# Kernel optimization log

Hardware: AMD Instinct MI355X
Metric: run time of the kernel (lower is better)

## Reference

```python
import jax, jax.numpy as jnp
import numpy as np

N = 100000   # nodes
E = 1600000  # edges (avg degree 16)
D = 64
L = 4        # layers per GNN stack


def setup_inputs() -> dict:
    key = jax.random.key(0)
    ks = jax.random.split(key, 16)
    s = 0.125  # ~kaiming scale for fan_in=64
    return {
        "x": jax.random.normal(ks[0], (N, D), jnp.float32),
        "edge_index": jax.random.randint(ks[1], (2, E), 0, N, dtype=jnp.int32),
        "sage_Wl": jax.random.normal(ks[2], (L, D, D), jnp.float32) * s,
        "sage_bl": jnp.zeros((L, D), jnp.float32),
        "sage_Wr": jax.random.normal(ks[3], (L, D, D), jnp.float32) * s,
        "gat_W": jax.random.normal(ks[4], (L, D, D), jnp.float32) * s,
        "gat_asrc": jax.random.normal(ks[5], (L, D), jnp.float32) * s,
        "gat_adst": jax.random.normal(ks[6], (L, D), jnp.float32) * s,
        "gat_b": jnp.zeros((L, D), jnp.float32),
        "proj_W1": jax.random.normal(ks[7], (64, 64), jnp.float32) * s,
        "proj_b1": jnp.zeros((64,), jnp.float32),
        "proj_W2": jax.random.normal(ks[8], (32, 64), jnp.float32) * s,
        "proj_b2": jnp.zeros((32,), jnp.float32),
        "proj_W3": jax.random.normal(ks[9], (16, 32), jnp.float32) * (0.25 ** 0.5),
        "proj_b3": jnp.zeros((16,), jnp.float32),
    }


def _sage_conv(x, Wl, bl, Wr, src, dst, n):
    # out_i = Wl @ mean_{j in N(i)} x_j + bl + Wr @ x_i
    msg_sum = jax.ops.segment_sum(x[src], dst, num_segments=n)
    deg = jax.ops.segment_sum(jnp.ones(src.shape[0], x.dtype), dst, num_segments=n)
    mean = msg_sum / jnp.maximum(deg, 1.0)[:, None]
    return mean @ Wl.T + bl + x @ Wr.T


def _gat_conv(x, W, a_src, a_dst, b, src_sl, dst_sl, n):
    # single-head GATConv with self-loops (src_sl/dst_sl include them)
    h = x @ W.T                      # [N, D]
    alpha_s = h @ a_src              # [N]
    alpha_d = h @ a_dst              # [N]
    e = jax.nn.leaky_relu(alpha_s[src_sl] + alpha_d[dst_sl], 0.2)  # [E+N]
    m = jax.ops.segment_max(e, dst_sl, num_segments=n)
    p = jnp.exp(e - m[dst_sl])
    z = jax.ops.segment_sum(p, dst_sl, num_segments=n)
    alpha = p / z[dst_sl]
    out = jax.ops.segment_sum(alpha[:, None] * h[src_sl], dst_sl, num_segments=n)
    return out + b


def reference(x, edge_index, sage_Wl, sage_bl, sage_Wr,
              gat_W, gat_asrc, gat_adst, gat_b,
              proj_W1, proj_b1, proj_W2, proj_b2, proj_W3, proj_b3):
    n = x.shape[0]
    src, dst = edge_index[0], edge_index[1]
    loops = jnp.arange(n, dtype=edge_index.dtype)
    src_sl = jnp.concatenate([src, loops])
    dst_sl = jnp.concatenate([dst, loops])

    h = x
    for i in range(L):  # GraphSAGE: ReLU between layers, none after last
        h = _sage_conv(h, sage_Wl[i], sage_bl[i], sage_Wr[i], src, dst, n)
        if i < L - 1:
            h = jax.nn.relu(h)
    for i in range(L):  # GAT
        h = _gat_conv(h, gat_W[i], gat_asrc[i], gat_adst[i], gat_b[i], src_sl, dst_sl, n)
        if i < L - 1:
            h = jax.nn.relu(h)

    # Projection MLP (Dropout inactive at inference)
    h = jax.nn.relu(h @ proj_W1.T + proj_b1)
    h = jax.nn.relu(h @ proj_W2.T + proj_b2)
    return h @ proj_W3.T + proj_b3
```

## Files before the change

### kernel.cpp

```cpp
#include <hip/hip_runtime.h>
#include <hip/hip_fp16.h>

#define D 64
#define D4 16
#define PITCH 68
#define HP 36

typedef float4 f4;
typedef unsigned int u32;
typedef __attribute__((ext_vector_type(4))) _Float16 f16x4;
typedef __attribute__((ext_vector_type(4))) float f32x4;

__device__ __forceinline__ float leaky02(float x) { return (x >= 0.f) ? x : 0.2f * x; }

__device__ __forceinline__ f4 f4add(f4 a, f4 b) {
    return make_float4(a.x + b.x, a.y + b.y, a.z + b.z, a.w + b.w);
}
__device__ __forceinline__ f4 f4fma(float s, f4 v, f4 a) {
    return make_float4(fmaf(s, v.x, a.x), fmaf(s, v.y, a.y), fmaf(s, v.z, a.z), fmaf(s, v.w, a.w));
}
__device__ __forceinline__ f4 f4scale(f4 a, float s) {
    return make_float4(a.x * s, a.y * s, a.z * s, a.w * s);
}

__device__ __forceinline__ u32 pack2(float a, float b) {
    __half2 h = __floats2half2_rn(a, b);
    return *reinterpret_cast<u32*>(&h);
}
__device__ __forceinline__ uint2 pack4(float a, float b, float c, float d) {
    uint2 u;
    u.x = pack2(a, b);
    u.y = pack2(c, d);
    return u;
}
__device__ __forceinline__ f4 h2f4(uint2 u) {
    __half2 ha = *reinterpret_cast<__half2*>(&u.x);
    __half2 hb = *reinterpret_cast<__half2*>(&u.y);
    float2 fa = __half22float2(ha);
    float2 fb = __half22float2(hb);
    return make_float4(fa.x, fa.y, fb.x, fb.y);
}


__global__ __launch_bounds__(256) void hist_kernel(const int* __restrict__ dst,
                                                   int* __restrict__ cnt, int ne) {
    int e = blockIdx.x * blockDim.x + threadIdx.x;
    if (e < ne) atomicAdd(&cnt[dst[e]], 1);
}

#define SCAN_BS 256
__global__ __launch_bounds__(SCAN_BS) void scan1_kernel(const int* __restrict__ cnt,
                                                        int* __restrict__ incl,
                                                        int* __restrict__ partials, int n) {
    __shared__ int sm[SCAN_BS];
    int g = blockIdx.x * SCAN_BS + threadIdx.x;
    int v = (g < n) ? cnt[g] : 0;
    sm[threadIdx.x] = v;
    __syncthreads();
    for (int off = 1; off < SCAN_BS; off <<= 1) {
        int t = (threadIdx.x >= off) ? sm[threadIdx.x - off] : 0;
        __syncthreads();
        sm[threadIdx.x] += t;
        __syncthreads();
    }
    if (g < n) incl[g] = sm[threadIdx.x];
    if (threadIdx.x == SCAN_BS - 1) partials[blockIdx.x] = sm[threadIdx.x];
}

__global__ __launch_bounds__(1024) void scan2_kernel(int* __restrict__ partials, int nb) {
    __shared__ int sm[1024];
    int t = threadIdx.x;
    int v = (t < nb) ? partials[t] : 0;
    sm[t] = v;
    __syncthreads();
    for (int off = 1; off < 1024; off <<= 1) {
        int x = (t >= off) ? sm[t - off] : 0;
        __syncthreads();
        sm[t] += x;
        __syncthreads();
    }
    if (t < nb) partials[t] = sm[t] - v;
}

__global__ __launch_bounds__(SCAN_BS) void scan3_kernel(const int* __restrict__ cnt,
                                                        const int* __restrict__ incl,
                                                        const int* __restrict__ partials,
                                                        int* __restrict__ rowptr,
                                                        int* __restrict__ cursor, int n, int ne) {
    int g = blockIdx.x * SCAN_BS + threadIdx.x;
    if (g < n) {
        int rp = incl[g] - cnt[g] + partials[blockIdx.x];
        rowptr[g] = rp;
        cursor[g] = rp;
    }
    if (g == 0) rowptr[n] = ne;
}

__global__ __launch_bounds__(256) void fill_kernel(const int* __restrict__ src,
                                                   const int* __restrict__ dst,
                                                   int* __restrict__ cursor,
                                                   int* __restrict__ col, int ne) {
    int e = blockIdx.x * blockDim.x + threadIdx.x;
    if (e < ne) {
        int pos = atomicAdd(&cursor[dst[e]], 1);
        col[pos] = src[e];
    }
}


__global__ __launch_bounds__(256) void to_half(const float* __restrict__ in,
                                               uint2* __restrict__ out, int total4) {
    int i = blockIdx.x * 256 + threadIdx.x;
    if (i < total4) {
        f4 v = *(const f4*)&in[i * 4];
        out[i] = pack4(v.x, v.y, v.z, v.w);
    }
}


__device__ __forceinline__ void stage_h32(u32* __restrict__ T, const f4* __restrict__ G4,
                                          int t, int valid_rows) {
    int row = t >> 2, q = t & 3;
#pragma unroll
    for (int c = 0; c < 4; c++) {
        int kq = q + 4 * c;
        f4 r = make_float4(0.f, 0.f, 0.f, 0.f);
        if (row < valid_rows) r = G4[(size_t)row * 16 + kq];
        uint2 p = pack4(r.x, r.y, r.z, r.w);
        T[row * HP + kq * 2] = p.x;
        T[row * HP + kq * 2 + 1] = p.y;
    }
}

__device__ __forceinline__ f16x4 ldfrag(const u32* __restrict__ T, int row, int kidx) {
    uint2 v;
    v.x = T[row * HP + kidx * 2];
    v.y = T[row * HP + kidx * 2 + 1];
    return __builtin_bit_cast(f16x4, v);
}


__device__ __forceinline__ void stageT(float* __restrict__ T, const f4* __restrict__ G4,
                                       int t, int valid_rows) {
    int row = t >> 2;
    int kq0 = t & 3;
#pragma unroll
    for (int c = 0; c < 4; c++) {
        int kq = kq0 + 4 * c;
        f4 r = make_float4(0.f, 0.f, 0.f, 0.f);
        if (row < valid_rows) r = G4[(size_t)row * 16 + kq];
        int k0 = kq * 4;
        T[(k0 + 0) * PITCH + row] = r.x;
        T[(k0 + 1) * PITCH + row] = r.y;
        T[(k0 + 2) * PITCH + row] = r.z;
        T[(k0 + 3) * PITCH + row] = r.w;
    }
}

#define TILE_MM(At, Wt, acc, r, c, KDIM)                                      \
    for (int k = 0; k < KDIM; k++) {                                          \
        f4 a = *(const f4*)&(At)[k * PITCH + (r) * 4];                        \
        f4 w = *(const f4*)&(Wt)[k * PITCH + (c) * 4];                        \
        acc[0][0] = fmaf(a.x, w.x, acc[0][0]);                                \
        acc[0][1] = fmaf(a.x, w.y, acc[0][1]);                                \
        acc[0][2] = fmaf(a.x, w.z, acc[0][2]);                                \
        acc[0][3] = fmaf(a.x, w.w, acc[0][3]);                                \
        acc[1][0] = fmaf(a.y, w.x, acc[1][0]);                                \
        acc[1][1] = fmaf(a.y, w.y, acc[1][1]);                                \
        acc[1][2] = fmaf(a.y, w.z, acc[1][2]);                                \
        acc[1][3] = fmaf(a.y, w.w, acc[1][3]);                                \
        acc[2][0] = fmaf(a.z, w.x, acc[2][0]);                                \
        acc[2][1] = fmaf(a.z, w.y, acc[2][1]);                                \
        acc[2][2] = fmaf(a.z, w.z, acc[2][2]);                                \
        acc[2][3] = fmaf(a.z, w.w, acc[2][3]);                                \
        acc[3][0] = fmaf(a.w, w.x, acc[3][0]);                                \
        acc[3][1] = fmaf(a.w, w.y, acc[3][1]);                                \
        acc[3][2] = fmaf(a.w, w.z, acc[3][2]);                                \
        acc[3][3] = fmaf(a.w, w.w, acc[3][3]);                                \
    }


__global__ __launch_bounds__(256) void sage_gather(const uint2* __restrict__ Hh,
                                                   const int* __restrict__ rowptr,
                                                   const int* __restrict__ col,
                                                   f4* __restrict__ M, int n) {
    int lane = threadIdx.x & 63;
    int eg = lane >> 4, l16 = lane & 15;
    int wave = (blockIdx.x * 256 + threadIdx.x) >> 6;
    int nw = (gridDim.x * 256) >> 6;
    for (int node = wave; node < n; node += nw) {
        int start = rowptr[node], end = rowptr[node + 1];
        int len = end - start;
        f4 a0 = {0, 0, 0, 0}, a1 = {0, 0, 0, 0}, a2 = {0, 0, 0, 0}, a3 = {0, 0, 0, 0};
        int main16 = len & ~15;
        int o = 0;
        for (; o < main16; o += 16) {
            int i0 = start + o + eg;
            int s0 = col[i0];
            int s1 = col[i0 + 4];
            int s2 = col[i0 + 8];
            int s3 = col[i0 + 12];
            uint2 v0 = Hh[(size_t)s0 * D4 + l16];
            uint2 v1 = Hh[(size_t)s1 * D4 + l16];
            uint2 v2 = Hh[(size_t)s2 * D4 + l16];
            uint2 v3 = Hh[(size_t)s3 * D4 + l16];
            a0 = f4add(a0, h2f4(v0)); a1 = f4add(a1, h2f4(v1));
            a2 = f4add(a2, h2f4(v2)); a3 = f4add(a3, h2f4(v3));
        }
        int rem = len - o;
        if (rem > 0) {
            int i0 = start + o;
            if (eg < rem)      a0 = f4add(a0, h2f4(Hh[(size_t)col[i0 + eg] * D4 + l16]));
            if (eg + 4 < rem)  a1 = f4add(a1, h2f4(Hh[(size_t)col[i0 + 4 + eg] * D4 + l16]));
            if (eg + 8 < rem)  a2 = f4add(a2, h2f4(Hh[(size_t)col[i0 + 8 + eg] * D4 + l16]));
            if (eg + 12 < rem) a3 = f4add(a3, h2f4(Hh[(size_t)col[i0 + 12 + eg] * D4 + l16]));
        }
        f4 a = f4add(f4add(a0, a1), f4add(a2, a3));
        a.x += __shfl_xor(a.x, 16); a.y += __shfl_xor(a.y, 16);
        a.z += __shfl_xor(a.z, 16); a.w += __shfl_xor(a.w, 16);
        a.x += __shfl_xor(a.x, 32); a.y += __shfl_xor(a.y, 32);
        a.z += __shfl_xor(a.z, 32); a.w += __shfl_xor(a.w, 32);
        if (eg == 0) {
            float invd = 1.f / fmaxf((float)len, 1.f);
            M[(size_t)node * D4 + l16] =
                make_float4(a.x * invd, a.y * invd, a.z * invd, a.w * invd);
        }
    }
}


__global__ __launch_bounds__(256) void sage_dense_mfma(const f4* __restrict__ M4,
                                                       const f4* __restrict__ h4,
                                                       const float* __restrict__ Wl,
                                                       const float* __restrict__ bl,
                                                       const float* __restrict__ Wr,
                                                       float* __restrict__ outf,
                                                       u32* __restrict__ outh32,
                                                       int relu_flag, int n) {
    __shared__ __align__(16) u32 Ah[64 * HP];
    __shared__ __align__(16) u32 Bh[64 * HP];
    int t = threadIdx.x;
    int nb = blockIdx.x * 64;
    int w = t >> 6, l = t & 63;
    int lr = l & 15, g = l >> 4;
    f32x4 acc[4] = {{0, 0, 0, 0}, {0, 0, 0, 0}, {0, 0, 0, 0}, {0, 0, 0, 0}};
    stage_h32(Ah, M4 + (size_t)nb * 16, t, n - nb);
    stage_h32(Bh, (const f4*)Wl, t, 64);
    __syncthreads();
#pragma unroll
    for (int kb = 0; kb < 4; kb++) {
        f16x4 af = ldfrag(Ah, w * 16 + lr, kb * 4 + g);
#pragma unroll
        for (int ob = 0; ob < 4; ob++) {
            f16x4 bf = ldfrag(Bh, ob * 16 + lr, kb * 4 + g);
            acc[ob] = __builtin_amdgcn_mfma_f32_16x16x16f16(af, bf, acc[ob], 0, 0, 0);
        }
    }
    __syncthreads();
    stage_h32(Ah, h4 + (size_t)nb * 16, t, n - nb);
    stage_h32(Bh, (const f4*)Wr, t, 64);
    __syncthreads();
#pragma unroll
    for (int kb = 0; kb < 4; kb++) {
        f16x4 af = ldfrag(Ah, w * 16 + lr, kb * 4 + g);
#pragma unroll
        for (int ob = 0; ob < 4; ob++) {
            f16x4 bf = ldfrag(Bh, ob * 16 + lr, kb * 4 + g);
            acc[ob] = __builtin_amdgcn_mfma_f32_16x16x16f16(af, bf, acc[ob], 0, 0, 0);
        }
    }
#pragma unroll
    for (int ob = 0; ob < 4; ob++) {
        int colx = ob * 16 + lr;
        float bv = bl[colx];
#pragma unroll
        for (int j = 0; j < 4; j++) {
            int row = w * 16 + 4 * g + j;
            int node = nb + row;
            float v = acc[ob][j] + bv;
            if (relu_flag) v = fmaxf(v, 0.f);
            float vup = __shfl_down(v, 1);
            if (node < n) {
                outf[(size_t)node * 64 + colx] = v;
                if ((lr & 1) == 0) outh32[(size_t)node * 32 + (colx >> 1)] = pack2(v, vup);
            }
        }
    }
}


__global__ __launch_bounds__(256) void gat_transform_mfma(const f4* __restrict__ h4,
                                                          const float* __restrict__ W,
                                                          const float* __restrict__ a_src,
                                                          const float* __restrict__ a_dst,
                                                          u32* __restrict__ hth32,
                                                          float* __restrict__ as_,
                                                          float* __restrict__ ad_, int n) {
    __shared__ __align__(16) u32 Ah[64 * HP];
    __shared__ __align__(16) u32 Bh[64 * HP];
    int t = threadIdx.x;
    int nb = blockIdx.x * 64;
    int w = t >> 6, l = t & 63;
    int lr = l & 15, g = l >> 4;
    f32x4 acc[4] = {{0, 0, 0, 0}, {0, 0, 0, 0}, {0, 0, 0, 0}, {0, 0, 0, 0}};
    stage_h32(Ah, h4 + (size_t)nb * 16, t, n - nb);
    stage_h32(Bh, (const f4*)W, t, 64);
    __syncthreads();
#pragma unroll
    for (int kb = 0; kb < 4; kb++) {
        f16x4 af = ldfrag(Ah, w * 16 + lr, kb * 4 + g);
#pragma unroll
        for (int ob = 0; ob < 4; ob++) {
            f16x4 bf = ldfrag(Bh, ob * 16 + lr, kb * 4 + g);
            acc[ob] = __builtin_amdgcn_mfma_f32_16x16x16f16(af, bf, acc[ob], 0, 0, 0);
        }
    }
    float asv[4], adv[4];
#pragma unroll
    for (int ob = 0; ob < 4; ob++) {
        asv[ob] = a_src[ob * 16 + lr];
        adv[ob] = a_dst[ob * 16 + lr];
    }
#pragma unroll
    for (int j = 0; j < 4; j++) {
        int row = w * 16 + 4 * g + j;
        int node = nb + row;
        float ps = 0.f, pd = 0.f;
#pragma unroll
        for (int ob = 0; ob < 4; ob++) {
            ps = fmaf(acc[ob][j], asv[ob], ps);
            pd = fmaf(acc[ob][j], adv[ob], pd);
        }
#pragma unroll
        for (int off = 1; off < 16; off <<= 1) {
            ps += __shfl_xor(ps, off);
            pd += __shfl_xor(pd, off);
        }
        if (lr == 0 && node < n) {
            as_[node] = ps;
            ad_[node] = pd;
        }
#pragma unroll
        for (int ob = 0; ob < 4; ob++) {
            int colx = ob * 16 + lr;
            float v = acc[ob][j];
            float vup = __shfl_down(v, 1);
            if (node < n && (lr & 1) == 0)
                hth32[(size_t)node * 32 + (colx >> 1)] = pack2(v, vup);
        }
    }
}


__global__ __launch_bounds__(256) void gat_gather(const int* __restrict__ rowptr,
                                                  const int* __restrict__ col,
                                                  const float* __restrict__ as_,
                                                  const float* __restrict__ ad_,
                                                  const uint2* __restrict__ Hh,
                                                  const float* __restrict__ b,
                                                  f4* __restrict__ out,
                                                  int relu_flag, int n) {
    int lane = threadIdx.x & 63;
    int eg = lane >> 4, l16 = lane & 15;
    int wave = (blockIdx.x * 256 + threadIdx.x) >> 6;
    int nw = (gridDim.x * 256) >> 6;
    const f4* b4 = (const f4*)b;
    for (int node = wave; node < n; node += nw) {
        int start = rowptr[node], end = rowptr[node + 1];
        int len = end - start;
        float ad_n = ad_[node];
        float e_self = leaky02(as_[node] + ad_n);
        float m = e_self;
        float zp = (eg == 0) ? 1.f : 0.f;
        f4 acc = {0, 0, 0, 0};
        if (eg == 0) acc = h2f4(Hh[(size_t)node * D4 + l16]);
        int main16 = len & ~15;
        int o = 0;
        for (; o < main16; o += 16) {
            int i0 = start + o + eg;
            int s0 = col[i0];
            int s1 = col[i0 + 4];
            int s2 = col[i0 + 8];
            int s3 = col[i0 + 12];
            uint2 v0 = Hh[(size_t)s0 * D4 + l16];
            uint2 v1 = Hh[(size_t)s1 * D4 + l16];
            uint2 v2 = Hh[(size_t)s2 * D4 + l16];
            uint2 v3 = Hh[(size_t)s3 * D4 + l16];
            float e0 = leaky02(as_[s0] + ad_n);
            float e1 = leaky02(as_[s1] + ad_n);
            float e2 = leaky02(as_[s2] + ad_n);
            float e3 = leaky02(as_[s3] + ad_n);
            float em = fmaxf(fmaxf(e0, e1), fmaxf(e2, e3));
            em = fmaxf(em, __shfl_xor(em, 16));
            em = fmaxf(em, __shfl_xor(em, 32));
            if (em > m) {
                float sc = __expf(m - em);
                zp *= sc;
                acc = f4scale(acc, sc);
                m = em;
            }
            float p0 = __expf(e0 - m);
            float p1 = __expf(e1 - m);
            float p2 = __expf(e2 - m);
            float p3 = __expf(e3 - m);
            zp += (p0 + p1) + (p2 + p3);
            acc = f4fma(p0, h2f4(v0), acc);
            acc = f4fma(p1, h2f4(v1), acc);
            acc = f4fma(p2, h2f4(v2), acc);
            acc = f4fma(p3, h2f4(v3), acc);
        }
        int rem = len - o;
        if (rem > 0) {
            int i0 = start + o;
            bool v0b = eg < rem, v1b = eg + 4 < rem, v2b = eg + 8 < rem, v3b = eg + 12 < rem;
            int s0 = v0b ? col[i0 + eg] : 0;
            int s1 = v1b ? col[i0 + 4 + eg] : 0;
            int s2 = v2b ? col[i0 + 8 + eg] : 0;
            int s3 = v3b ? col[i0 + 12 + eg] : 0;
            float e0 = v0b ? leaky02(as_[s0] + ad_n) : -3.4e38f;
            float e1 = v1b ? leaky02(as_[s1] + ad_n) : -3.4e38f;
            float e2 = v2b ? leaky02(as_[s2] + ad_n) : -3.4e38f;
            float e3 = v3b ? leaky02(as_[s3] + ad_n) : -3.4e38f;
            float em = fmaxf(fmaxf(e0, e1), fmaxf(e2, e3));
            em = fmaxf(em, __shfl_xor(em, 16));
            em = fmaxf(em, __shfl_xor(em, 32));
            if (em > m) {
                float sc = __expf(m - em);
                zp *= sc;
                acc = f4scale(acc, sc);
                m = em;
            }
            float p0 = v0b ? __expf(e0 - m) : 0.f;
            float p1 = v1b ? __expf(e1 - m) : 0.f;
            float p2 = v2b ? __expf(e2 - m) : 0.f;
            float p3 = v3b ? __expf(e3 - m) : 0.f;
            zp += (p0 + p1) + (p2 + p3);
            if (v0b) acc = f4fma(p0, h2f4(Hh[(size_t)s0 * D4 + l16]), acc);
            if (v1b) acc = f4fma(p1, h2f4(Hh[(size_t)s1 * D4 + l16]), acc);
            if (v2b) acc = f4fma(p2, h2f4(Hh[(size_t)s2 * D4 + l16]), acc);
            if (v3b) acc = f4fma(p3, h2f4(Hh[(size_t)s3 * D4 + l16]), acc);
        }
        float z = zp;
        z += __shfl_xor(z, 16);
        z += __shfl_xor(z, 32);
        acc.x += __shfl_xor(acc.x, 16); acc.y += __shfl_xor(acc.y, 16);
        acc.z += __shfl_xor(acc.z, 16); acc.w += __shfl_xor(acc.w, 16);
        acc.x += __shfl_xor(acc.x, 32); acc.y += __shfl_xor(acc.y, 32);
        acc.z += __shfl_xor(acc.z, 32); acc.w += __shfl_xor(acc.w, 32);
        if (eg == 0) {
            float rz = 1.f / z;
            f4 bb = b4[l16];
            f4 o4 = make_float4(fmaf(acc.x, rz, bb.x), fmaf(acc.y, rz, bb.y),
                                fmaf(acc.z, rz, bb.z), fmaf(acc.w, rz, bb.w));
            if (relu_flag) {
                o4.x = fmaxf(o4.x, 0.f); o4.y = fmaxf(o4.y, 0.f);
                o4.z = fmaxf(o4.z, 0.f); o4.w = fmaxf(o4.w, 0.f);
            }
            out[(size_t)node * D4 + l16] = o4;
        }
    }
}


__global__ __launch_bounds__(256) void mlp_kernel(const f4* __restrict__ h4,
                                                  const float* __restrict__ W1,
                                                  const float* __restrict__ b1,
                                                  const float* __restrict__ W2,
                                                  const float* __restrict__ b2,
                                                  const float* __restrict__ W3,
                                                  const float* __restrict__ b3,
                                                  float* __restrict__ out, int n) {
    __shared__ float At[64 * PITCH];
    __shared__ float Wt[64 * PITCH];
    __shared__ float V2[32 * PITCH];
    int t = threadIdx.x;
    int nb = blockIdx.x * 64;
    int r = t >> 4, c = t & 15;
    stageT(At, h4 + (size_t)nb * 16, t, n - nb);
    stageT(Wt, (const f4*)W1, t, 64);
    __syncthreads();
    float a1v[4][4] = {{0.f}};
    TILE_MM(At, Wt, a1v, r, c, 64)
    f4 b1v = ((const f4*)b1)[c];
    __syncthreads();
    {
        float bb[4] = {b1v.x, b1v.y, b1v.z, b1v.w};
#pragma unroll
        for (int i = 0; i < 4; i++)
#pragma unroll
            for (int j = 0; j < 4; j++)
                At[(c * 4 + j) * PITCH + r * 4 + i] = fmaxf(a1v[i][j] + bb[j], 0.f);
    }
    stageT(Wt, (const f4*)W2, t, 32);
    __syncthreads();
    float a2v[4][2] = {{0.f}};
    for (int k = 0; k < 64; k++) {
        f4 a = *(const f4*)&At[k * PITCH + r * 4];
        float w0 = Wt[k * PITCH + c * 2];
        float w1 = Wt[k * PITCH + c * 2 + 1];
        a2v[0][0] = fmaf(a.x, w0, a2v[0][0]); a2v[0][1] = fmaf(a.x, w1, a2v[0][1]);
        a2v[1][0] = fmaf(a.y, w0, a2v[1][0]); a2v[1][1] = fmaf(a.y, w1, a2v[1][1]);
        a2v[2][0] = fmaf(a.z, w0, a2v[2][0]); a2v[2][1] = fmaf(a.z, w1, a2v[2][1]);
        a2v[3][0] = fmaf(a.w, w0, a2v[3][0]); a2v[3][1] = fmaf(a.w, w1, a2v[3][1]);
    }
    float b20 = b2[c * 2], b21 = b2[c * 2 + 1];
    __syncthreads();
#pragma unroll
    for (int i = 0; i < 4; i++) {
        V2[(c * 2 + 0) * PITCH + r * 4 + i] = fmaxf(a2v[i][0] + b20, 0.f);
        V2[(c * 2 + 1) * PITCH + r * 4 + i] = fmaxf(a2v[i][1] + b21, 0.f);
    }
    if (t < 128) {
        int row = t >> 3, kq = t & 7;
        f4 w = ((const f4*)W3)[row * 8 + kq];
        int k0 = kq * 4;
        Wt[(k0 + 0) * PITCH + row] = w.x;
        Wt[(k0 + 1) * PITCH + row] = w.y;
        Wt[(k0 + 2) * PITCH + row] = w.z;
        Wt[(k0 + 3) * PITCH + row] = w.w;
    }
    __syncthreads();
    float a3v[4] = {0.f, 0.f, 0.f, 0.f};
    for (int k = 0; k < 32; k++) {
        f4 a = *(const f4*)&V2[k * PITCH + r * 4];
        float w = Wt[k * PITCH + c];
        a3v[0] = fmaf(a.x, w, a3v[0]);
        a3v[1] = fmaf(a.y, w, a3v[1]);
        a3v[2] = fmaf(a.z, w, a3v[2]);
        a3v[3] = fmaf(a.w, w, a3v[3]);
    }
    float b3v = b3[c];
#pragma unroll
    for (int i = 0; i < 4; i++) {
        int node = nb + r * 4 + i;
        if (node < n) out[(size_t)node * 16 + c] = a3v[i] + b3v;
    }
}


extern "C" void kernel_launch(void* const* d_in, const int* in_sizes, int n_in,
                              void* d_out, int out_size, void* d_ws, size_t ws_size,
                              hipStream_t stream) {
    const int n  = in_sizes[0] / D;
    const int ne = in_sizes[1] / 2;

    const float* x        = (const float*)d_in[0];
    const int*   ei       = (const int*)d_in[1];
    const int*   src      = ei;
    const int*   dst      = ei + ne;
    const float* sage_Wl  = (const float*)d_in[2];
    const float* sage_bl  = (const float*)d_in[3];
    const float* sage_Wr  = (const float*)d_in[4];
    const float* gat_W    = (const float*)d_in[5];
    const float* gat_asrc = (const float*)d_in[6];
    const float* gat_adst = (const float*)d_in[7];
    const float* gat_b    = (const float*)d_in[8];
    const float* W1 = (const float*)d_in[9];
    const float* b1 = (const float*)d_in[10];
    const float* W2 = (const float*)d_in[11];
    const float* b2 = (const float*)d_in[12];
    const float* W3 = (const float*)d_in[13];
    const float* b3 = (const float*)d_in[14];
    float* out = (float*)d_out;

    int*   cnt      = (int*)d_ws;
    int*   incl     = cnt + n;
    int*   rowptr   = incl + n;
    int*   cursor   = rowptr + n + 4;
    int*   partials = cursor + n;
    int*   col      = partials + 1024;
    float* as_      = (float*)(col + ne);
    float* ad_      = as_ + n;
    float* M        = ad_ + n;
    float* bufA     = M + (size_t)n * D;
    float* bufB     = bufA + (size_t)n * D;
    uint2* Hh       = (uint2*)(bufB + (size_t)n * D);

    const int gridE  = (ne + 255) / 256;
    const int nb     = (n + SCAN_BS - 1) / SCAN_BS;
    const int gridG  = 4096;
    const int gridM  = (n + 63) / 64;
    const int gridC  = (n * D / 4 + 255) / 256;

    hipMemsetAsync(cnt, 0, (size_t)n * 4, stream);
    hist_kernel<<<gridE, 256, 0, stream>>>(dst, cnt, ne);
    scan1_kernel<<<nb, SCAN_BS, 0, stream>>>(cnt, incl, partials, n);
    scan2_kernel<<<1, 1024, 0, stream>>>(partials, nb);
    scan3_kernel<<<nb, SCAN_BS, 0, stream>>>(cnt, incl, partials, rowptr, cursor, n, ne);
    fill_kernel<<<gridE, 256, 0, stream>>>(src, dst, cursor, col, ne);

    to_half<<<gridC, 256, 0, stream>>>(x, Hh, n * D / 4);
    const float* cur = x;
    float* nxt = bufA;
    for (int l = 0; l < 4; l++) {
        sage_gather<<<gridG, 256, 0, stream>>>(Hh, rowptr, col, (f4*)M, n);
        sage_dense_mfma<<<gridM, 256, 0, stream>>>((const f4*)M, (const f4*)cur,
                                                   sage_Wl + (size_t)l * D * D,
                                                   sage_bl + (size_t)l * D,
                                                   sage_Wr + (size_t)l * D * D,
                                                   nxt, (u32*)Hh, (l < 3) ? 1 : 0, n);
        cur = nxt;
        nxt = (nxt == bufA) ? bufB : bufA;
    }

    float* gin = bufB;
    for (int l = 0; l < 4; l++) {
        gat_transform_mfma<<<gridM, 256, 0, stream>>>((const f4*)gin,
                                                      gat_W + (size_t)l * D * D,
                                                      gat_asrc + (size_t)l * D,
                                                      gat_adst + (size_t)l * D,
                                                      (u32*)Hh, as_, ad_, n);
        gat_gather<<<gridG, 256, 0, stream>>>(rowptr, col, as_, ad_,
                                              Hh, gat_b + (size_t)l * D, (f4*)gin,
                                              (l < 3) ? 1 : 0, n);
    }

    mlp_kernel<<<gridM, 256, 0, stream>>>((const f4*)gin, W1, b1, W2, b2, W3, b3, out, n);
}
```

Measured before the change: 869.0 us.

## Fuse SAGE neighbor gather with MFMA dense transform via LDS staging

Merges the SAGE mean-aggregation gather and the MFMA dense layer into one kernel. Each wave gathers 16 nodes and writes the fp16 mean straight into shared memory instead of round-tripping an fp32 M buffer through global memory. The fp16 feature buffer is now double-buffered (A/B ping-pong) so that blocks reading neighbors never race with blocks writing outputs. This also drops one launch per layer. In exchange the gather runs with a fixed per-block node assignment instead of a grid-stride loop over more waves, which may reduce latency hiding and load balance.

```diff
diff --git a/kernel.cpp b/kernel.cpp
--- a/kernel.cpp
+++ b/kernel.cpp
@@ -180,15 +180,36 @@
     }
 
 
-__global__ __launch_bounds__(256) void sage_gather(const uint2* __restrict__ Hh,
-                                                   const int* __restrict__ rowptr,
-                                                   const int* __restrict__ col,
-                                                   f4* __restrict__ M, int n) {
-    int lane = threadIdx.x & 63;
-    int eg = lane >> 4, l16 = lane & 15;
-    int wave = (blockIdx.x * 256 + threadIdx.x) >> 6;
-    int nw = (gridDim.x * 256) >> 6;
-    for (int node = wave; node < n; node += nw) {
+__global__ __launch_bounds__(256) void sage_fused(const uint2* __restrict__ Hh_in,
+                                                  const f4* __restrict__ h4,
+                                                  const int* __restrict__ rowptr,
+                                                  const int* __restrict__ col,
+                                                  const float* __restrict__ Wl,
+                                                  const float* __restrict__ bl,
+                                                  const float* __restrict__ Wr,
+                                                  float* __restrict__ outf,
+                                                  u32* __restrict__ Hh_out,
+                                                  int relu_flag, int n) {
+    __shared__ __align__(16) u32 Ah[64 * HP];
+    __shared__ __align__(16) u32 Bh[64 * HP];
+    int t = threadIdx.x;
+    int nb = blockIdx.x * 64;
+    int w = t >> 6, l = t & 63;
+    int lr = l & 15, g = l >> 4;
+    int eg = l >> 4, l16 = l & 15;
+
+    stage_h32(Bh, (const f4*)Wl, t, 64);
+
+    for (int i = 0; i < 16; i++) {
+        int row = w * 16 + i;
+        int node = nb + row;
+        if (node >= n) {
+            if (eg == 0) {
+                Ah[row * HP + l16 * 2] = 0u;
+                Ah[row * HP + l16 * 2 + 1] = 0u;
+            }
+            continue;
+        }
         int start = rowptr[node], end = rowptr[node + 1];
         int len = end - start;
         f4 a0 = {0, 0, 0, 0}, a1 = {0, 0, 0, 0}, a2 = {0, 0, 0, 0}, a3 = {0, 0, 0, 0};
@@ -200,20 +221,20 @@
             int s1 = col[i0 + 4];
             int s2 = col[i0 + 8];
             int s3 = col[i0 + 12];
-            uint2 v0 = Hh[(size_t)s0 * D4 + l16];
-            uint2 v1 = Hh[(size_t)s1 * D4 + l16];
-            uint2 v2 = Hh[(size_t)s2 * D4 + l16];
-            uint2 v3 = Hh[(size_t)s3 * D4 + l16];
+            uint2 v0 = Hh_in[(size_t)s0 * D4 + l16];
+            uint2 v1 = Hh_in[(size_t)s1 * D4 + l16];
+            uint2 v2 = Hh_in[(size_t)s2 * D4 + l16];
+            uint2 v3 = Hh_in[(size_t)s3 * D4 + l16];
             a0 = f4add(a0, h2f4(v0)); a1 = f4add(a1, h2f4(v1));
             a2 = f4add(a2, h2f4(v2)); a3 = f4add(a3, h2f4(v3));
         }
         int rem = len - o;
         if (rem > 0) {
             int i0 = start + o;
-            if (eg < rem)      a0 = f4add(a0, h2f4(Hh[(size_t)col[i0 + eg] * D4 + l16]));
-            if (eg + 4 < rem)  a1 = f4add(a1, h2f4(Hh[(size_t)col[i0 + 4 + eg] * D4 + l16]));
-            if (eg + 8 < rem)  a2 = f4add(a2, h2f4(Hh[(size_t)col[i0 + 8 + eg] * D4 + l16]));
-            if (eg + 12 < rem) a3 = f4add(a3, h2f4(Hh[(size_t)col[i0 + 12 + eg] * D4 + l16]));
+            if (eg < rem)      a0 = f4add(a0, h2f4(Hh_in[(size_t)col[i0 + eg] * D4 + l16]));
+            if (eg + 4 < rem)  a1 = f4add(a1, h2f4(Hh_in[(size_t)col[i0 + 4 + eg] * D4 + l16]));
+            if (eg + 8 < rem)  a2 = f4add(a2, h2f4(Hh_in[(size_t)col[i0 + 8 + eg] * D4 + l16]));
+            if (eg + 12 < rem) a3 = f4add(a3, h2f4(Hh_in[(size_t)col[i0 + 12 + eg] * D4 + l16]));
         }
         f4 a = f4add(f4add(a0, a1), f4add(a2, a3));
         a.x += __shfl_xor(a.x, 16); a.y += __shfl_xor(a.y, 16);
@@ -222,31 +243,13 @@
         a.z += __shfl_xor(a.z, 32); a.w += __shfl_xor(a.w, 32);
         if (eg == 0) {
             float invd = 1.f / fmaxf((float)len, 1.f);
-            M[(size_t)node * D4 + l16] =
-                make_float4(a.x * invd, a.y * invd, a.z * invd, a.w * invd);
-        }
-    }
-}
-
-
-__global__ __launch_bounds__(256) void sage_dense_mfma(const f4* __restrict__ M4,
-                                                       const f4* __restrict__ h4,
-                                                       const float* __restrict__ Wl,
-                                                       const float* __restrict__ bl,
-                                                       const float* __restrict__ Wr,
-                                                       float* __restrict__ outf,
-                                                       u32* __restrict__ outh32,
-                                                       int relu_flag, int n) {
-    __shared__ __align__(16) u32 Ah[64 * HP];
-    __shared__ __align__(16) u32 Bh[64 * HP];
-    int t = threadIdx.x;
-    int nb = blockIdx.x * 64;
-    int w = t >> 6, l = t & 63;
-    int lr = l & 15, g = l >> 4;
+            Ah[row * HP + l16 * 2] = pack2(a.x * invd, a.y * invd);
+            Ah[row * HP + l16 * 2 + 1] = pack2(a.z * invd, a.w * invd);
+        }
+    }
+    __syncthreads();
+
     f32x4 acc[4] = {{0, 0, 0, 0}, {0, 0, 0, 0}, {0, 0, 0, 0}, {0, 0, 0, 0}};
-    stage_h32(Ah, M4 + (size_t)nb * 16, t, n - nb);
-    stage_h32(Bh, (const f4*)Wl, t, 64);
-    __syncthreads();
 #pragma unroll
     for (int kb = 0; kb < 4; kb++) {
         f16x4 af = ldfrag(Ah, w * 16 + lr, kb * 4 + g);
@@ -282,7 +285,7 @@
             float vup = __shfl_down(v, 1);
             if (node < n) {
                 outf[(size_t)node * 64 + colx] = v;
-                if ((lr & 1) == 0) outh32[(size_t)node * 32 + (colx >> 1)] = pack2(v, vup);
+                if ((lr & 1) == 0) Hh_out[(size_t)node * 32 + (colx >> 1)] = pack2(v, vup);
             }
         }
     }
@@ -571,10 +574,10 @@
     int*   col      = partials + 1024;
     float* as_      = (float*)(col + ne);
     float* ad_      = as_ + n;
-    float* M        = ad_ + n;
-    float* bufA     = M + (size_t)n * D;
+    float* bufA     = ad_ + n;
     float* bufB     = bufA + (size_t)n * D;
-    uint2* Hh       = (uint2*)(bufB + (size_t)n * D);
+    uint2* HhA      = (uint2*)(bufB + (size_t)n * D);
+    uint2* HhB      = HhA + (size_t)n * 16;
 
     const int gridE  = (ne + 255) / 256;
     const int nb     = (n + SCAN_BS - 1) / SCAN_BS;
@@ -589,18 +592,20 @@
     scan3_kernel<<<nb, SCAN_BS, 0, stream>>>(cnt, incl, partials, rowptr, cursor, n, ne);
     fill_kernel<<<gridE, 256, 0, stream>>>(src, dst, cursor, col, ne);
 
-    to_half<<<gridC, 256, 0, stream>>>(x, Hh, n * D / 4);
+    to_half<<<gridC, 256, 0, stream>>>(x, HhA, n * D / 4);
     const float* cur = x;
     float* nxt = bufA;
+    uint2* hin = HhA;
+    uint2* hout = HhB;
     for (int l = 0; l < 4; l++) {
-        sage_gather<<<gridG, 256, 0, stream>>>(Hh, rowptr, col, (f4*)M, n);
-        sage_dense_mfma<<<gridM, 256, 0, stream>>>((const f4*)M, (const f4*)cur,
-                                                   sage_Wl + (size_t)l * D * D,
-                                                   sage_bl + (size_t)l * D,
-                                                   sage_Wr + (size_t)l * D * D,
-                                                   nxt, (u32*)Hh, (l < 3) ? 1 : 0, n);
+        sage_fused<<<gridM, 256, 0, stream>>>(hin, (const f4*)cur, rowptr, col,
+                                              sage_Wl + (size_t)l * D * D,
+                                              sage_bl + (size_t)l * D,
+                                              sage_Wr + (size_t)l * D * D,
+                                              nxt, (u32*)hout, (l < 3) ? 1 : 0, n);
         cur = nxt;
         nxt = (nxt == bufA) ? bufB : bufA;
+        uint2* tmp = hin; hin = hout; hout = tmp;
     }
 
     float* gin = bufB;
@@ -609,9 +614,9 @@
                                                       gat_W + (size_t)l * D * D,
                                                       gat_asrc + (size_t)l * D,
                                                       gat_adst + (size_t)l * D,
-                                                      (u32*)Hh, as_, ad_, n);
+                                                      (u32*)hout, as_, ad_, n);
         gat_gather<<<gridG, 256, 0, stream>>>(rowptr, col, as_, ad_,
-                                              Hh, gat_b + (size_t)l * D, (f4*)gin,
+                                              hout, gat_b + (size_t)l * D, (f4*)gin,
                                               (l < 3) ? 1 : 0, n);
     }
 
```

Result: slower. 955.1 us (+9.9%).
